# Kernel tuning notes

Hardware: AMD Instinct MI355X
Metric: run time of the kernel (lower is better)

The kernel has to match this reference:

```python
import jax, jax.numpy as jnp
import numpy as np

D_MODEL = 2048
N_HEADS = 16
N_KV_HEADS = 4
HEAD_DIM = 128
ROPE_THETA = 1000000.0
B, T = 2, 2048


def setup_inputs() -> dict:
    key = jax.random.key(0)
    ks = jax.random.split(key, 5)
    s_in = 1.0 / np.sqrt(D_MODEL)
    s_o = 1.0 / np.sqrt(N_HEADS * HEAD_DIM)
    return {
        "x": jax.random.normal(ks[0], (B, T, D_MODEL), jnp.float32),
        "w_q": jax.random.normal(ks[1], (N_HEADS * HEAD_DIM, D_MODEL), jnp.float32) * s_in,
        "w_k": jax.random.normal(ks[2], (N_KV_HEADS * HEAD_DIM, D_MODEL), jnp.float32) * s_in,
        "w_v": jax.random.normal(ks[3], (N_KV_HEADS * HEAD_DIM, D_MODEL), jnp.float32) * s_in,
        "w_o": jax.random.normal(ks[4], (D_MODEL, N_HEADS * HEAD_DIM), jnp.float32) * s_o,
    }


def _rope_cos_sin(T, dtype):
    # inv_freq over even dims, emb = concat(freqs, freqs) (HF/llama convention)
    inv_freq = 1.0 / (ROPE_THETA ** (jnp.arange(0, HEAD_DIM, 2, dtype=jnp.float32) / HEAD_DIM))
    freqs = jnp.arange(T, dtype=jnp.float32)[:, None] * inv_freq[None, :]  # [T, hd/2]
    emb = jnp.concatenate([freqs, freqs], axis=-1)  # [T, hd]
    return jnp.cos(emb).astype(dtype), jnp.sin(emb).astype(dtype)


def _rotate_half(x):
    x1, x2 = jnp.split(x, 2, axis=-1)
    return jnp.concatenate([-x2, x1], axis=-1)


def reference(x, w_q, w_k, w_v, w_o):
    B, T, D = x.shape
    # QKV projections (bias=False), split heads -> [B, H, T, hd]
    q = (x @ w_q.T).reshape(B, T, N_HEADS, HEAD_DIM).transpose(0, 2, 1, 3)
    k = (x @ w_k.T).reshape(B, T, N_KV_HEADS, HEAD_DIM).transpose(0, 2, 1, 3)
    v = (x @ w_v.T).reshape(B, T, N_KV_HEADS, HEAD_DIM).transpose(0, 2, 1, 3)
    # RoPE
    cos, sin = _rope_cos_sin(T, x.dtype)  # [T, hd]
    q = q * cos + _rotate_half(q) * sin
    k = k * cos + _rotate_half(k) * sin
    # GQA: expand kv heads (repeat_interleave over head dim)
    rep = N_HEADS // N_KV_HEADS
    k = jnp.repeat(k, rep, axis=1)
    v = jnp.repeat(v, rep, axis=1)
    # Eager attention: QK^T * scale + causal mask, softmax, PV
    scale = HEAD_DIM ** -0.5
    scores = jnp.einsum("bhtd,bhsd->bhts", q, k) * scale
    causal = jnp.tril(jnp.ones((T, T), dtype=bool))
    scores = jnp.where(causal[None, None], scores, jnp.finfo(scores.dtype).min)
    probs = jax.nn.softmax(scores, axis=-1)
    out = jnp.einsum("bhts,bhsd->bhtd", probs, v)  # [B, H, T, hd]
    out = out.transpose(0, 2, 1, 3).reshape(B, T, N_HEADS * HEAD_DIM)
    return out @ w_o.T
```

## Files before the change

### kernel.cpp

```cpp
#include <hip/hip_runtime.h>
#include <cstdint>
#include <cstddef>

typedef unsigned short u16;
typedef unsigned u32;
typedef unsigned long long u64;
typedef __attribute__((ext_vector_type(8))) short short8;
typedef __attribute__((ext_vector_type(4))) float f32x4;

#define T_SEQ 2048
#define DM    2048
#define NHEAD 16
#define NKV   4
#define HD    128
#define NEGBIG (-3.0e38f)
#define QSCALE 0.1275525165017459f
#define L2IF (-0.31143258583318043f)

__device__ __forceinline__ u16 f2bf(float f) {
  union { float f; unsigned u; } c; c.f = f;
  return (u16)((c.u + 0x7fffu + ((c.u >> 16) & 1u)) >> 16);
}
__device__ __forceinline__ float bf2f(u16 b) {
  union { float f; unsigned u; } c; c.u = ((unsigned)b) << 16;
  return c.f;
}
__device__ __forceinline__ void gl_lds16(const u16* g, u16* l) {
  __builtin_amdgcn_global_load_lds(
      (const __attribute__((address_space(1))) void*)g,
      (__attribute__((address_space(3))) void*)l, 16, 0, 0);
}

__global__ void castk_all(const float* __restrict__ x, const float* __restrict__ wq,
                          const float* __restrict__ wk, const float* __restrict__ wv,
                          const float* __restrict__ wo, u16* __restrict__ dst) {
  long long i4 = (long long)blockIdx.x * 256 + threadIdx.x;
  const float* src; long long off;
  if (i4 < (2LL << 20))                    { src = x;  off = i4; }
  else if (i4 < (3LL << 20))               { src = wq; off = i4 - (2LL << 20); }
  else if (i4 < (3LL << 20) + (1 << 18))   { src = wk; off = i4 - (3LL << 20); }
  else if (i4 < (3LL << 20) + (2 << 18))   { src = wv; off = i4 - (3LL << 20) - (1 << 18); }
  else                                     { src = wo; off = i4 - (3LL << 20) - (2 << 18); }
  float4 v = *(const float4*)(src + off * 4);
  u16* d = dst + i4 * 4;
  d[0] = f2bf(v.x); d[1] = f2bf(v.y); d[2] = f2bf(v.z); d[3] = f2bf(v.w);
}

__global__ void ropek(u16* __restrict__ buf) {
  int idx = blockIdx.x * 256 + threadIdx.x;
  int r = idx >> 6, i = idx & 63;
  int t = r & (T_SEQ - 1);
  float inv = exp2f((float)i * L2IF);
  float ang = (float)t * inv;
  float c = cosf(ang), s = sinf(ang);
  size_t base = (size_t)r * HD + i;
  float x1 = bf2f(buf[base]), x2 = bf2f(buf[base + 64]);
  buf[base]      = f2bf(x1 * c - x2 * s);
  buf[base + 64] = f2bf(x2 * c + x1 * s);
}

template <int MODE>
__global__ __launch_bounds__(256) void gemm_bt(
    const u16* __restrict__ A, const u16* __restrict__ Bm,
    void* __restrict__ Out0, u16* __restrict__ OutK, u16* __restrict__ OutV,
    int M, int N, int K) {
  __shared__ __align__(16) u16 As[2][128 * 32];
  __shared__ __align__(16) u16 Bs[2][128 * 32];
  const int tid = threadIdx.x;
  const int w = tid >> 6, l = tid & 63;
  const int lm = l & 15, q = l >> 4;
  const int m0 = blockIdx.y * 128, n0 = blockIdx.x * 128;
  const int mq = w & 1, nq = w >> 1;
  const u16* Ab = A + (size_t)m0 * K;
  const u16* Bb = Bm + (size_t)n0 * K;

  const int s0_ = w * 64 + l, s1_ = 256 + s0_;
  const int row0 = s0_ >> 2, kq0 = (s0_ & 3) * 8;
  const int row1 = s1_ >> 2, kq1 = (s1_ & 3) * 8;

  f32x4 acc[4][4] = {};
  const int nk = K >> 5;

  gl_lds16(Ab + (size_t)row0 * K + kq0, &As[0][s0_ * 8]);
  gl_lds16(Bb + (size_t)row0 * K + kq0, &Bs[0][s0_ * 8]);
  gl_lds16(Ab + (size_t)row1 * K + kq1, &As[0][s1_ * 8]);
  gl_lds16(Bb + (size_t)row1 * K + kq1, &Bs[0][s1_ * 8]);
  __syncthreads();

  for (int ki = 0; ki < nk; ++ki) {
    const int bb = ki & 1;
    if (ki + 1 < nk) {
      const int k0 = (ki + 1) << 5;
      gl_lds16(Ab + (size_t)row0 * K + k0 + kq0, &As[bb ^ 1][s0_ * 8]);
      gl_lds16(Bb + (size_t)row0 * K + k0 + kq0, &Bs[bb ^ 1][s0_ * 8]);
      gl_lds16(Ab + (size_t)row1 * K + k0 + kq1, &As[bb ^ 1][s1_ * 8]);
      gl_lds16(Bb + (size_t)row1 * K + k0 + kq1, &Bs[bb ^ 1][s1_ * 8]);
    }
    short8 af[4], bf[4];
#pragma unroll
    for (int i = 0; i < 4; ++i) {
      af[i] = *(const short8*)(&As[bb][(mq * 64 + i * 16 + lm) * 32 + q * 8]);
      bf[i] = *(const short8*)(&Bs[bb][(nq * 64 + i * 16 + lm) * 32 + q * 8]);
    }
#pragma unroll
    for (int i = 0; i < 4; ++i)
#pragma unroll
      for (int j = 0; j < 4; ++j)
        acc[i][j] = __builtin_amdgcn_mfma_f32_16x16x32_bf16(af[i], bf[j], acc[i][j], 0, 0, 0);
    __syncthreads();
  }

#pragma unroll
  for (int i = 0; i < 4; ++i)
#pragma unroll
    for (int j = 0; j < 4; ++j)
#pragma unroll
      for (int r = 0; r < 4; ++r) {
        int m = m0 + mq * 64 + i * 16 + q * 4 + r;
        int n = n0 + nq * 64 + j * 16 + lm;
        float v = acc[i][j][r];
        if constexpr (MODE == 0) {
          ((float*)Out0)[(size_t)m * N + n] = v;
        } else {
          int b = m >> 11, t = m & (T_SEQ - 1);
          if (n < 2048) {
            int h = n >> 7, d = n & (HD - 1);
            ((u16*)Out0)[(((size_t)(b * NHEAD + h)) * T_SEQ + t) * HD + d] = f2bf(v * QSCALE);
          } else if (n < 2560) {
            int nn = n - 2048, h = nn >> 7, d = nn & (HD - 1);
            OutK[(((size_t)(b * NKV + h)) * T_SEQ + t) * HD + d] = f2bf(v);
          } else {
            int nn = n - 2560, h = nn >> 7, d = nn & (HD - 1);
            OutV[(((size_t)(b * NKV + h)) * HD + d) * T_SEQ + t] = f2bf(v);
          }
        }
      }
}

#define PSTRIDE 72
__global__ __launch_bounds__(256, 2) void attnk(
    const u16* __restrict__ Q, const u16* __restrict__ Kh,
    const u16* __restrict__ Vt, u16* __restrict__ Oa) {
  __shared__ __align__(16) u16 Ks[2][64 * 128];
  __shared__ __align__(16) u16 Vs[2][128 * 64];
  __shared__ __align__(16) u16 Pl[4][16 * PSTRIDE];
  const int tid = threadIdx.x;
  const int w = tid >> 6, l = tid & 63, lm = l & 15, q = l >> 4;
  const int bh = blockIdx.y, b = bh >> 4, h = bh & 15, kvh = h >> 2;
  const u16* Kb = Kh + ((size_t)(b * NKV + kvh)) * T_SEQ * HD;
  const u16* Vb = Vt + ((size_t)(b * NKV + kvh)) * HD * T_SEQ;
  u16* Pw = Pl[w];
  const int p = blockIdx.x;

  const int r16 = tid >> 4, c16 = tid & 15;
  const int r8  = tid >> 3, c8  = tid & 7;

#pragma unroll 1
  for (int half = 0; half < 2; ++half) {
    const int tile = half ? p : (31 - p);
    const int tbase = tile * 64 + w * 16;
    const u16* Qb = Q + (((size_t)(b * NHEAD + h)) * T_SEQ + tbase) * HD;

    short8 qa[4];
#pragma unroll
    for (int ks = 0; ks < 4; ++ks)
      qa[ks] = *(const short8*)(Qb + (size_t)lm * HD + ks * 32 + q * 8);

    {
      const float tf = (float)(tbase + lm);
#pragma unroll
      for (int ks = 0; ks < 2; ++ks) {
        short8 lo = qa[ks], hi = qa[ks + 2];
#pragma unroll
        for (int e = 0; e < 8; ++e) {
          int d = ks * 32 + q * 8 + e;
          float ang = tf * exp2f((float)d * L2IF);
          float sn, cs;
          sincosf(ang, &sn, &cs);
          float x1 = bf2f((u16)lo[e]), x2 = bf2f((u16)hi[e]);
          lo[e] = (short)f2bf(x1 * cs - x2 * sn);
          hi[e] = (short)f2bf(x2 * cs + x1 * sn);
        }
        qa[ks] = lo; qa[ks + 2] = hi;
      }
    }

    float m_i = NEGBIG, l_i = 0.f;
    f32x4 oacc[8] = {};
    const int nst = tile + 1;

    {
#pragma unroll
      for (int j = 0; j < 4; ++j) {
        int s = j * 16 + r16, g = c16 ^ (s & 15);
        gl_lds16(Kb + (size_t)s * HD + g * 8, &Ks[0][s * 128 + c16 * 8]);
      }
#pragma unroll
      for (int j = 0; j < 4; ++j) {
        int d = j * 32 + r8, g = c8 ^ (d & 7);
        gl_lds16(Vb + (size_t)d * T_SEQ + g * 8, &Vs[0][d * 64 + c8 * 8]);
      }
    }
    __syncthreads();

    for (int st = 0; st < nst; ++st) {
      const int bb = st & 1;
      if (st + 1 < nst) {
        const int s0n = (st + 1) * 64;
#pragma unroll
        for (int j = 0; j < 4; ++j) {
          int s = j * 16 + r16, g = c16 ^ (s & 15);
          gl_lds16(Kb + (size_t)(s0n + s) * HD + g * 8, &Ks[bb ^ 1][s * 128 + c16 * 8]);
        }
#pragma unroll
        for (int j = 0; j < 4; ++j) {
          int d = j * 32 + r8, g = c8 ^ (d & 7);
          gl_lds16(Vb + (size_t)d * T_SEQ + s0n + g * 8, &Vs[bb ^ 1][d * 64 + c8 * 8]);
        }
      }

      f32x4 sacc[4] = {};
#pragma unroll
      for (int ks = 0; ks < 4; ++ks)
#pragma unroll
        for (int nt = 0; nt < 4; ++nt) {
          short8 kb = *(const short8*)(&Ks[bb][(nt * 16 + lm) * 128 + ((ks * 4 + q) ^ lm) * 8]);
          sacc[nt] = __builtin_amdgcn_mfma_f32_16x16x32_bf16(kb, qa[ks], sacc[nt], 0, 0, 0);
        }

      const bool diag = (st == nst - 1);
      const int s0 = st * 64;
      float mx = m_i;
      float pe[4][4];
#pragma unroll
      for (int nt = 0; nt < 4; ++nt)
#pragma unroll
        for (int j = 0; j < 4; ++j) {
          float v = sacc[nt][j];
          if (diag) {
            int s_abs = s0 + nt * 16 + q * 4 + j;
            if (s_abs > tbase + lm) v = NEGBIG;
          }
          pe[nt][j] = v;
          mx = fmaxf(mx, v);
        }
      mx = fmaxf(mx, __shfl_xor(mx, 16, 64));
      mx = fmaxf(mx, __shfl_xor(mx, 32, 64));
      float alpha = exp2f(m_i - mx);
      float sum = 0.f;
#pragma unroll
      for (int nt = 0; nt < 4; ++nt) {
        float e0 = exp2f(pe[nt][0] - mx), e1 = exp2f(pe[nt][1] - mx);
        float e2 = exp2f(pe[nt][2] - mx), e3 = exp2f(pe[nt][3] - mx);
        sum += (e0 + e1) + (e2 + e3);
        u32 lo32 = __builtin_amdgcn_perm(__float_as_uint(e1), __float_as_uint(e0), 0x07060302u);
        u32 hi32 = __builtin_amdgcn_perm(__float_as_uint(e3), __float_as_uint(e2), 0x07060302u);
        *(u64*)(Pw + lm * PSTRIDE + nt * 16 + q * 4) = ((u64)hi32 << 32) | lo32;
      }
      sum += __shfl_xor(sum, 16, 64);
      sum += __shfl_xor(sum, 32, 64);
      bool bump = (mx > m_i);
      m_i = mx;
      l_i = l_i * alpha + sum;

      if (__any(bump)) {
#pragma unroll
        for (int dt = 0; dt < 8; ++dt)
#pragma unroll
          for (int j = 0; j < 4; ++j) oacc[dt][j] *= alpha;
      }

      asm volatile("" ::: "memory");

#pragma unroll
      for (int ks = 0; ks < 2; ++ks) {
        short8 pa = *(const short8*)(Pw + lm * PSTRIDE + ks * 32 + q * 8);
#pragma unroll
        for (int dt = 0; dt < 8; ++dt) {
          short8 vb = *(const short8*)(
              &Vs[bb][(dt * 16 + lm) * 64 + ((ks * 4 + q) ^ (lm & 7)) * 8]);
          oacc[dt] = __builtin_amdgcn_mfma_f32_16x16x32_bf16(vb, pa, oacc[dt], 0, 0, 0);
        }
      }
      __syncthreads();
    }

    float inv = 1.0f / l_i;
    int t = tbase + lm;
#pragma unroll
    for (int dt = 0; dt < 8; ++dt) {
      u16 ok[4];
#pragma unroll
      for (int j = 0; j < 4; ++j) ok[j] = f2bf(oacc[dt][j] * inv);
      *(u64*)(Oa + ((size_t)(b * T_SEQ + t)) * (NHEAD * HD) + h * HD + dt * 16 + q * 4) =
          (u64)ok[0] | ((u64)ok[1] << 16) | ((u64)ok[2] << 32) | ((u64)ok[3] << 48);
    }
  }
}

extern "C" void kernel_launch(void* const* d_in, const int* in_sizes, int n_in,
                              void* d_out, int out_size, void* d_ws, size_t ws_size,
                              hipStream_t stream) {
  const float* x  = (const float*)d_in[0];
  const float* wq = (const float*)d_in[1];
  const float* wk = (const float*)d_in[2];
  const float* wv = (const float*)d_in[3];
  const float* wo = (const float*)d_in[4];
  float* out = (float*)d_out;

  u16* ws  = (u16*)d_ws;
  u16* xb  = ws;
  u16* wqb = xb  + (8u << 20);
  u16* wkb = wqb + (4u << 20);
  u16* wvb = wkb + (1u << 20);
  u16* wob = wvb + (1u << 20);
  u16* Qb  = wob + (4u << 20);
  u16* Kb  = Qb  + (8u << 20);
  u16* Vtb = Kb  + (2u << 20);
  u16* Ab  = xb;

  castk_all<<<18432, 256, 0, stream>>>(x, wq, wk, wv, wo, ws);

  gemm_bt<3><<<dim3(24, 32), 256, 0, stream>>>(xb, wqb, Qb, Kb, Vtb, 4096, 3072, 2048);

  ropek<<<4096, 256, 0, stream>>>(Kb);

  attnk<<<dim3(16, 32), 256, 0, stream>>>(Qb, Kb, Vtb, Ab);

  gemm_bt<0><<<dim3(16, 32), 256, 0, stream>>>(Ab, wob, out, nullptr, nullptr, 4096, 2048, 2048);
}
```

Baseline: 300.3 us.

## Precompute RoPE table, group attention blocks by KV head, lazy softmax rescale

Adds a kernel that builds a cos/sin table once, and uses it in both the K RoPE pass and the in-attention Q RoPE instead of computing transcendentals per element. Reorders the attention grid so blocks sharing a KV head are scheduled together, for better cache reuse of K/V. Changes the online softmax to rescale only when the running max grows by more than a threshold, skipping most rescale multiplies. This trades an extra table kernel and table loads for fewer transcendental ops, and slightly changes the numerics of the unnormalized probabilities.

Measured after the change: 295.2 us. Within noise of the previous version (-1.7%).

```diff
diff --git a/kernel.cpp b/kernel.cpp
--- a/kernel.cpp
+++ b/kernel.cpp
@@ -46,17 +46,23 @@
   d[0] = f2bf(v.x); d[1] = f2bf(v.y); d[2] = f2bf(v.z); d[3] = f2bf(v.w);
 }
 
-__global__ void ropek(u16* __restrict__ buf) {
+__global__ void tabk(float2* __restrict__ Tab) {
+  int idx = blockIdx.x * 256 + threadIdx.x;
+  float ang = (float)(idx >> 6) * exp2f((float)(idx & 63) * L2IF);
+  float sn, cs;
+  sincosf(ang, &sn, &cs);
+  Tab[idx] = make_float2(cs, sn);
+}
+
+__global__ void ropek(u16* __restrict__ buf, const float2* __restrict__ Tab) {
   int idx = blockIdx.x * 256 + threadIdx.x;
   int r = idx >> 6, i = idx & 63;
   int t = r & (T_SEQ - 1);
-  float inv = exp2f((float)i * L2IF);
-  float ang = (float)t * inv;
-  float c = cosf(ang), s = sinf(ang);
+  float2 cs = Tab[(t << 6) + i];
   size_t base = (size_t)r * HD + i;
   float x1 = bf2f(buf[base]), x2 = bf2f(buf[base + 64]);
-  buf[base]      = f2bf(x1 * c - x2 * s);
-  buf[base + 64] = f2bf(x2 * c + x1 * s);
+  buf[base]      = f2bf(x1 * cs.x - x2 * cs.y);
+  buf[base + 64] = f2bf(x2 * cs.x + x1 * cs.y);
 }
 
 template <int MODE>
@@ -140,17 +146,23 @@
 #define PSTRIDE 72
 __global__ __launch_bounds__(256, 2) void attnk(
     const u16* __restrict__ Q, const u16* __restrict__ Kh,
-    const u16* __restrict__ Vt, u16* __restrict__ Oa) {
+    const u16* __restrict__ Vt, const float2* __restrict__ Tab,
+    u16* __restrict__ Oa) {
   __shared__ __align__(16) u16 Ks[2][64 * 128];
   __shared__ __align__(16) u16 Vs[2][128 * 64];
   __shared__ __align__(16) u16 Pl[4][16 * PSTRIDE];
   const int tid = threadIdx.x;
   const int w = tid >> 6, l = tid & 63, lm = l & 15, q = l >> 4;
-  const int bh = blockIdx.y, b = bh >> 4, h = bh & 15, kvh = h >> 2;
+
+  const int wg = blockIdx.x;
+  const int g = wg & 7, slot = wg >> 3;
+  const int b = g >> 2, kvh = g & 3;
+  const int h = kvh * 4 + (slot & 3);
+  const int p = slot >> 2;
+
   const u16* Kb = Kh + ((size_t)(b * NKV + kvh)) * T_SEQ * HD;
   const u16* Vb = Vt + ((size_t)(b * NKV + kvh)) * HD * T_SEQ;
   u16* Pw = Pl[w];
-  const int p = blockIdx.x;
 
   const int r16 = tid >> 4, c16 = tid & 15;
   const int r8  = tid >> 3, c8  = tid & 7;
@@ -167,19 +179,16 @@
       qa[ks] = *(const short8*)(Qb + (size_t)lm * HD + ks * 32 + q * 8);
 
     {
-      const float tf = (float)(tbase + lm);
+      const float2* tb = Tab + (((size_t)(tbase + lm)) << 6) + q * 8;
 #pragma unroll
       for (int ks = 0; ks < 2; ++ks) {
         short8 lo = qa[ks], hi = qa[ks + 2];
 #pragma unroll
         for (int e = 0; e < 8; ++e) {
-          int d = ks * 32 + q * 8 + e;
-          float ang = tf * exp2f((float)d * L2IF);
-          float sn, cs;
-          sincosf(ang, &sn, &cs);
+          float2 cs = tb[ks * 32 + e];
           float x1 = bf2f((u16)lo[e]), x2 = bf2f((u16)hi[e]);
-          lo[e] = (short)f2bf(x1 * cs - x2 * sn);
-          hi[e] = (short)f2bf(x2 * cs + x1 * sn);
+          lo[e] = (short)f2bf(x1 * cs.x - x2 * cs.y);
+          hi[e] = (short)f2bf(x2 * cs.x + x1 * cs.y);
         }
         qa[ks] = lo; qa[ks + 2] = hi;
       }
@@ -192,13 +201,13 @@
     {
 #pragma unroll
       for (int j = 0; j < 4; ++j) {
-        int s = j * 16 + r16, g = c16 ^ (s & 15);
-        gl_lds16(Kb + (size_t)s * HD + g * 8, &Ks[0][s * 128 + c16 * 8]);
+        int s = j * 16 + r16, gs = c16 ^ (s & 15);
+        gl_lds16(Kb + (size_t)s * HD + gs * 8, &Ks[0][s * 128 + c16 * 8]);
       }
 #pragma unroll
       for (int j = 0; j < 4; ++j) {
-        int d = j * 32 + r8, g = c8 ^ (d & 7);
-        gl_lds16(Vb + (size_t)d * T_SEQ + g * 8, &Vs[0][d * 64 + c8 * 8]);
+        int d = j * 32 + r8, gs = c8 ^ (d & 7);
+        gl_lds16(Vb + (size_t)d * T_SEQ + gs * 8, &Vs[0][d * 64 + c8 * 8]);
       }
     }
     __syncthreads();
@@ -209,13 +218,13 @@
         const int s0n = (st + 1) * 64;
 #pragma unroll
         for (int j = 0; j < 4; ++j) {
-          int s = j * 16 + r16, g = c16 ^ (s & 15);
-          gl_lds16(Kb + (size_t)(s0n + s) * HD + g * 8, &Ks[bb ^ 1][s * 128 + c16 * 8]);
+          int s = j * 16 + r16, gs = c16 ^ (s & 15);
+          gl_lds16(Kb + (size_t)(s0n + s) * HD + gs * 8, &Ks[bb ^ 1][s * 128 + c16 * 8]);
         }
 #pragma unroll
         for (int j = 0; j < 4; ++j) {
-          int d = j * 32 + r8, g = c8 ^ (d & 7);
-          gl_lds16(Vb + (size_t)d * T_SEQ + s0n + g * 8, &Vs[bb ^ 1][d * 64 + c8 * 8]);
+          int d = j * 32 + r8, gs = c8 ^ (d & 7);
+          gl_lds16(Vb + (size_t)d * T_SEQ + s0n + gs * 8, &Vs[bb ^ 1][d * 64 + c8 * 8]);
         }
       }
 
@@ -230,8 +239,7 @@
 
       const bool diag = (st == nst - 1);
       const int s0 = st * 64;
-      float mx = m_i;
-      float pe[4][4];
+      float mx = NEGBIG;
 #pragma unroll
       for (int nt = 0; nt < 4; ++nt)
 #pragma unroll
@@ -240,18 +248,27 @@
           if (diag) {
             int s_abs = s0 + nt * 16 + q * 4 + j;
             if (s_abs > tbase + lm) v = NEGBIG;
+            sacc[nt][j] = v;
           }
-          pe[nt][j] = v;
           mx = fmaxf(mx, v);
         }
       mx = fmaxf(mx, __shfl_xor(mx, 16, 64));
       mx = fmaxf(mx, __shfl_xor(mx, 32, 64));
-      float alpha = exp2f(m_i - mx);
+      if (__any(mx > m_i + 8.0f)) {
+        float mnew = fmaxf(m_i, mx);
+        float alpha = exp2f(m_i - mnew);
+        m_i = mnew;
+        l_i *= alpha;
+#pragma unroll
+        for (int dt = 0; dt < 8; ++dt)
+#pragma unroll
+          for (int j = 0; j < 4; ++j) oacc[dt][j] *= alpha;
+      }
       float sum = 0.f;
 #pragma unroll
       for (int nt = 0; nt < 4; ++nt) {
-        float e0 = exp2f(pe[nt][0] - mx), e1 = exp2f(pe[nt][1] - mx);
-        float e2 = exp2f(pe[nt][2] - mx), e3 = exp2f(pe[nt][3] - mx);
+        float e0 = exp2f(sacc[nt][0] - m_i), e1 = exp2f(sacc[nt][1] - m_i);
+        float e2 = exp2f(sacc[nt][2] - m_i), e3 = exp2f(sacc[nt][3] - m_i);
         sum += (e0 + e1) + (e2 + e3);
         u32 lo32 = __builtin_amdgcn_perm(__float_as_uint(e1), __float_as_uint(e0), 0x07060302u);
         u32 hi32 = __builtin_amdgcn_perm(__float_as_uint(e3), __float_as_uint(e2), 0x07060302u);
@@ -259,16 +276,7 @@
       }
       sum += __shfl_xor(sum, 16, 64);
       sum += __shfl_xor(sum, 32, 64);
-      bool bump = (mx > m_i);
-      m_i = mx;
-      l_i = l_i * alpha + sum;
-
-      if (__any(bump)) {
-#pragma unroll
-        for (int dt = 0; dt < 8; ++dt)
-#pragma unroll
-          for (int j = 0; j < 4; ++j) oacc[dt][j] *= alpha;
-      }
+      l_i += sum;
 
       asm volatile("" ::: "memory");
 
@@ -318,14 +326,16 @@
   u16* Kb  = Qb  + (8u << 20);
   u16* Vtb = Kb  + (2u << 20);
   u16* Ab  = xb;
+  float2* tab = (float2*)wkb;
 
   castk_all<<<18432, 256, 0, stream>>>(x, wq, wk, wv, wo, ws);
 
   gemm_bt<3><<<dim3(24, 32), 256, 0, stream>>>(xb, wqb, Qb, Kb, Vtb, 4096, 3072, 2048);
 
-  ropek<<<4096, 256, 0, stream>>>(Kb);
-
-  attnk<<<dim3(16, 32), 256, 0, stream>>>(Qb, Kb, Vtb, Ab);
+  tabk<<<512, 256, 0, stream>>>(tab);
+  ropek<<<4096, 256, 0, stream>>>(Kb, tab);
+
+  attnk<<<512, 256, 0, stream>>>(Qb, Kb, Vtb, tab, Ab);
 
   gemm_bt<0><<<dim3(16, 32), 256, 0, stream>>>(Ab, wob, out, nullptr, nullptr, 4096, 2048, 2048);
 }
```
